# Kernel tuning notes

Hardware: AMD Instinct MI355X
Metric: run time of the kernel (lower is better)

## Reference

```python
import jax, jax.numpy as jnp
import numpy as np

B, N, S, VC, P, E, H = 8, 1024, 64, 8, 3, 64, 4
HD = E // H


def setup_inputs() -> dict:
    key = jax.random.key(0)
    ks = jax.random.split(key, 20)
    def rn(k, shape, scale=1.0):
        return jax.random.normal(k, shape, dtype=jnp.float32) * scale
    inp = {
        "s": rn(ks[0], (B, N, S)),
        "v": rn(ks[1], (B, N, VC, 3)),
        "coords": rn(ks[2], (B, N, 3)),
        # p-adic encoder: Linear(1,16) -> SiLU -> Linear(16, 64)
        "enc_w1": rn(ks[3], (16, 1), 1.0),
        "enc_b1": jnp.zeros((16,), jnp.float32),
        "enc_w2": rn(ks[4], (S, 16), 1.0 / np.sqrt(16)),
        "enc_b2": jnp.zeros((S,), jnp.float32),
        # 3 GVP layers, all with s_cat dim 72 -> s_out 64, v 8 -> 8
        "scal_w": rn(ks[5], (3, S, S + VC), 1.0 / np.sqrt(S + VC)),
        "scal_b": jnp.zeros((3, S), jnp.float32),
        "vec_w": rn(ks[6], (3, VC, VC), 1.0 / np.sqrt(VC)),
        "gate_w": rn(ks[7], (3, VC, S + VC), 1.0 / np.sqrt(S + VC)),
        "gate_b": jnp.zeros((3, VC), jnp.float32),
        # MultiheadAttention (embed 64, 4 heads)
        "in_proj_w": rn(ks[8], (3 * E, E), 1.0 / np.sqrt(E)),
        "in_proj_b": jnp.zeros((3 * E,), jnp.float32),
        "out_proj_w": rn(ks[9], (E, E), 1.0 / np.sqrt(E)),
        "out_proj_b": jnp.zeros((E,), jnp.float32),
    }
    return inp


def _padic_distance(coords):
    # pairwise diffs (B, N, N, 3)
    diff = coords[:, :, None, :] - coords[:, None, :, :]
    di = (jnp.abs(diff) * 1000.0).astype(jnp.int32)
    # valuation = max k in [1,10] with p^k | di  == count of divisible k (divisibility chain)
    cnt = jnp.zeros(di.shape, jnp.int32)
    for k in range(1, 11):
        cnt = cnt + (di % (P ** k) == 0).astype(jnp.int32)
    val = jnp.where(di > 0, cnt, 0).astype(jnp.float32).mean(-1)  # (B,N,N)
    return jnp.float32(P) ** (-val)


def reference(s, v, coords, enc_w1, enc_b1, enc_w2, enc_b2,
              scal_w, scal_b, vec_w, gate_w, gate_b,
              in_proj_w, in_proj_b, out_proj_w, out_proj_b):
    silu = jax.nn.silu
    pd = _padic_distance(coords)  # (B,N,N)
    pf = silu(pd.mean(-1, keepdims=True) @ enc_w1.T + enc_b1) @ enc_w2.T + enc_b2
    s = s + pf

    for i in range(3):
        act = i < 2  # last layer has no activations (gate always applied)
        vn = jnp.linalg.norm(v, axis=-1)               # (B,N,VC)
        sc = jnp.concatenate([s, vn], axis=-1)         # (B,N,S+VC)
        s_new = sc @ scal_w[i].T + scal_b[i]
        if act:
            s_new = silu(s_new)
        v_new = jnp.einsum('oi,bnix->bnox', vec_w[i], v)
        if act:
            v_new = v_new * jax.nn.sigmoid(jnp.linalg.norm(v_new, axis=-1, keepdims=True))
        gate = jax.nn.sigmoid(sc @ gate_w[i].T + gate_b[i])
        v_new = v_new * gate[..., None]
        if i > 0:
            s, v = s + s_new, v + v_new
        else:
            s, v = s_new, v_new

    # p-adic biased multi-head attention (additive mask = -padic_dist per head)
    qkv = s @ in_proj_w.T + in_proj_b                 # (B,N,3E)
    q, k, vv = jnp.split(qkv, 3, axis=-1)
    q = q.reshape(B, N, H, HD)
    k = k.reshape(B, N, H, HD)
    vv = vv.reshape(B, N, H, HD)
    scores = jnp.einsum('bqhd,bkhd->bhqk', q, k) / np.sqrt(HD)
    scores = scores - pd[:, None, :, :]
    attn = jax.nn.softmax(scores, axis=-1)
    o = jnp.einsum('bhqk,bkhd->bqhd', attn, vv).reshape(B, N, E)
    s = s + (o @ out_proj_w.T + out_proj_b)

    return s, v, pd
```

## Files before the change

### kernel.cpp

```cpp
#include <hip/hip_runtime.h>
#include <hip/hip_bf16.h>
#include <math.h>

#define BB 8
#define NN 1024
#define SS 64
#define VCC 8
#define EE 64
#define HH 4
#define HDD 16

#define OUT_S_OFF 0
#define OUT_V_OFF 524288
#define OUT_PD_OFF 720896

__device__ __forceinline__ int val3(int d) {
    int c = 0;
    unsigned ud = (unsigned)d;
    c += (ud % 3u == 0u);
    c += (ud % 9u == 0u);
    c += (ud % 27u == 0u);
    c += (ud % 81u == 0u);
    c += (ud % 243u == 0u);
    c += (ud % 729u == 0u);
    c += (ud % 2187u == 0u);
    c += (ud % 6561u == 0u);
    c += (ud % 19683u == 0u);
    c += (ud % 59049u == 0u);
    return d > 0 ? c : 0;
}

__device__ __forceinline__ float silu_f(float x) {
    return x / (1.0f + expf(-x));
}
__device__ __forceinline__ float sigmoid_f(float x) {
    return 1.0f / (1.0f + expf(-x));
}

#define IR 16
__global__ __launch_bounds__(256) void pd_kernel(const float* __restrict__ coords,
                                                 float* __restrict__ pd_out,
                                                 float* __restrict__ pdmean) {
    const int bi = blockIdx.x;
    const int b = bi >> 6;
    const int ibase = (bi & 63) * IR;
    const int tid = threadIdx.x;
    const float* cb = coords + (size_t)b * NN * 3;

    __shared__ float sx[1024];
    __shared__ float sy[1024];
    __shared__ float sz[1024];
    __shared__ float red[IR][4];

    for (int idx = tid; idx < 3072; idx += 256) {
        float v = cb[idx];
        int j = idx / 3;
        int c = idx - j * 3;
        float* dst = (c == 0) ? sx : (c == 1) ? sy : sz;
        dst[j] = v;
    }
    __syncthreads();

    const int j0 = tid * 4;
    float4 x4 = *(const float4*)&sx[j0];
    float4 y4 = *(const float4*)&sy[j0];
    float4 z4 = *(const float4*)&sz[j0];
    float xs[4] = {x4.x, x4.y, x4.z, x4.w};
    float ys[4] = {y4.x, y4.y, y4.z, y4.w};
    float zs[4] = {z4.x, z4.y, z4.z, z4.w};

    const float kLog2_3_over3 = 0.5283208335737187f;

    for (int ii = 0; ii < IR; ++ii) {
        const int i = ibase + ii;
        const float cx = sx[i], cy = sy[i], cz = sz[i];
        float p[4];
        float lsum = 0.0f;
        #pragma unroll
        for (int t = 0; t < 4; ++t) {
            int d0 = (int)(fabsf(cx - xs[t]) * 1000.0f);
            int d1 = (int)(fabsf(cy - ys[t]) * 1000.0f);
            int d2 = (int)(fabsf(cz - zs[t]) * 1000.0f);
            int cnt = val3(d0) + val3(d1) + val3(d2);
            p[t] = exp2f(-(float)cnt * kLog2_3_over3);
            lsum += p[t];
        }
        *(float4*)&pd_out[((size_t)(b * NN + i)) * NN + j0] =
            make_float4(p[0], p[1], p[2], p[3]);
        float x = lsum;
        #pragma unroll
        for (int off = 32; off > 0; off >>= 1) x += __shfl_xor(x, off, 64);
        if ((tid & 63) == 0) red[ii][tid >> 6] = x;
    }
    __syncthreads();
    if (tid < IR) {
        pdmean[b * NN + ibase + tid] =
            (red[tid][0] + red[tid][1] + red[tid][2] + red[tid][3]) * (1.0f / 1024.0f);
    }
}

#define GR 4
__global__ __launch_bounds__(64) void gvp_kernel(const float* __restrict__ s_in,
                           const float* __restrict__ v_in,
                           const float* __restrict__ enc_w1,
                           const float* __restrict__ enc_b1,
                           const float* __restrict__ enc_w2,
                           const float* __restrict__ enc_b2,
                           const float* __restrict__ scal_w,
                           const float* __restrict__ scal_b,
                           const float* __restrict__ vec_w,
                           const float* __restrict__ gate_w,
                           const float* __restrict__ gate_b,
                           const float* __restrict__ pdmean,
                           float* __restrict__ s_gvp,
                           float* __restrict__ v_out) {
    const int lane = threadIdx.x;
    const int rbase = blockIdx.x * GR;

    __shared__ float sc[GR][80];
    __shared__ float vbuf[GR][24];
    __shared__ float vtb[GR][24];
    __shared__ float gg[GR][8];
    __shared__ float hid[GR][16];

    #pragma unroll
    for (int r = 0; r < GR; ++r) {
        const int row = rbase + r;
        sc[r][lane] = s_in[(size_t)row * 64 + lane];
        if (lane < 24) vbuf[r][lane] = v_in[(size_t)row * 24 + lane];
        if (lane < 16) {
            float pm = pdmean[row];
            hid[r][lane] = silu_f(pm * enc_w1[lane] + enc_b1[lane]);
        }
    }
    __syncthreads();
    #pragma unroll
    for (int r = 0; r < GR; ++r) {
        float acc = enc_b2[lane];
        #pragma unroll
        for (int h = 0; h < 16; ++h) acc += hid[r][h] * enc_w2[lane * 16 + h];
        sc[r][lane] += acc;
    }
    __syncthreads();

    for (int layer = 0; layer < 3; ++layer) {
        const bool act = layer < 2;
        if (lane < 8) {
            #pragma unroll
            for (int r = 0; r < GR; ++r) {
                float x = vbuf[r][lane * 3 + 0];
                float y = vbuf[r][lane * 3 + 1];
                float z = vbuf[r][lane * 3 + 2];
                sc[r][64 + lane] = sqrtf(x * x + y * y + z * z);
            }
        }
        __syncthreads();

        float sn[GR];
        {
            float4 w4[18];
            const float4* wr = (const float4*)(scal_w + ((size_t)layer * 64 + lane) * 72);
            #pragma unroll
            for (int k = 0; k < 18; ++k) w4[k] = wr[k];
            const float sb = scal_b[layer * 64 + lane];
            #pragma unroll
            for (int r = 0; r < GR; ++r) {
                const float4* sv = (const float4*)sc[r];
                float acc = sb;
                #pragma unroll
                for (int k = 0; k < 18; ++k) {
                    float4 s4 = sv[k];
                    acc += w4[k].x * s4.x + w4[k].y * s4.y + w4[k].z * s4.z + w4[k].w * s4.w;
                }
                sn[r] = acc;
            }
        }
        if (lane < 8) {
            float4 g4[18];
            const float4* gr_ = (const float4*)(gate_w + ((size_t)layer * 8 + lane) * 72);
            #pragma unroll
            for (int k = 0; k < 18; ++k) g4[k] = gr_[k];
            const float gb = gate_b[layer * 8 + lane];
            #pragma unroll
            for (int r = 0; r < GR; ++r) {
                const float4* sv = (const float4*)sc[r];
                float acc = gb;
                #pragma unroll
                for (int k = 0; k < 18; ++k) {
                    float4 s4 = sv[k];
                    acc += g4[k].x * s4.x + g4[k].y * s4.y + g4[k].z * s4.z + g4[k].w * s4.w;
                }
                gg[r][lane] = sigmoid_f(acc);
            }
        }
        if (lane < 24) {
            const int o = lane / 3;
            const int xc = lane - o * 3;
            const float* vw = vec_w + ((size_t)layer * 8 + o) * 8;
            float vwr[8];
            #pragma unroll
            for (int ii = 0; ii < 8; ++ii) vwr[ii] = vw[ii];
            #pragma unroll
            for (int r = 0; r < GR; ++r) {
                float acc = 0.0f;
                #pragma unroll
                for (int ii = 0; ii < 8; ++ii) acc += vwr[ii] * vbuf[r][ii * 3 + xc];
                vtb[r][lane] = acc;
            }
        }
        __syncthreads();

        #pragma unroll
        for (int r = 0; r < GR; ++r) {
            float val = act ? silu_f(sn[r]) : sn[r];
            sc[r][lane] = (layer > 0) ? (sc[r][lane] + val) : val;
        }
        if (lane < 24) {
            const int o = lane / 3;
            #pragma unroll
            for (int r = 0; r < GR; ++r) {
                float val = vtb[r][lane];
                if (act) {
                    float a = vtb[r][o * 3 + 0];
                    float bb2 = vtb[r][o * 3 + 1];
                    float c2 = vtb[r][o * 3 + 2];
                    val *= sigmoid_f(sqrtf(a * a + bb2 * bb2 + c2 * c2));
                }
                val *= gg[r][o];
                vbuf[r][lane] = (layer > 0) ? (vbuf[r][lane] + val) : val;
            }
        }
        __syncthreads();
    }

    #pragma unroll
    for (int r = 0; r < GR; ++r) {
        const int row = rbase + r;
        s_gvp[(size_t)row * 64 + lane] = sc[r][lane];
        if (lane < 24) v_out[(size_t)row * 24 + lane] = vbuf[r][lane];
    }
}

#define QROWS 8
__global__ __launch_bounds__(192) void qkv_kernel(const float* __restrict__ s_gvp,
                           const float* __restrict__ w,
                           const float* __restrict__ bias,
                           float* __restrict__ q,
                           float* __restrict__ k,
                           float* __restrict__ v) {
    const int tid = threadIdx.x;
    const int rbase = blockIdx.x * QROWS;
    __shared__ float sl[QROWS][64];
    for (int idx = tid; idx < QROWS * 64; idx += 192)
        sl[idx >> 6][idx & 63] = s_gvp[(size_t)rbase * 64 + idx];
    __syncthreads();

    float4 w4[16];
    const float4* wr = (const float4*)(w + (size_t)tid * 64);
    #pragma unroll
    for (int kk = 0; kk < 16; ++kk) w4[kk] = wr[kk];
    const float bv = bias[tid];

    const int which = tid >> 6;
    const int e = tid & 63;
    const int h = e >> 4, d = e & 15;
    float* dst = (which == 0) ? q : (which == 1) ? k : v;

    #pragma unroll
    for (int r = 0; r < QROWS; ++r) {
        const float4* sv = (const float4*)sl[r];
        float acc = bv;
        #pragma unroll
        for (int kk = 0; kk < 16; ++kk) {
            float4 s4 = sv[kk];
            acc += w4[kk].x * s4.x + w4[kk].y * s4.y + w4[kk].z * s4.z + w4[kk].w * s4.w;
        }
        const int row = rbase + r;
        const int b = row >> 10, n = row & 1023;
        dst[(((size_t)(b * HH + h)) * NN + n) * HDD + d] = acc;
    }
}

__global__ __launch_bounds__(256, 2)
void attn_kernel(const float* __restrict__ q,
                 const float* __restrict__ k,
                 const float* __restrict__ v,
                 const float* __restrict__ pd,
                 float* __restrict__ po,
                 float* __restrict__ pm,
                 float* __restrict__ pl) {
    const int ks = blockIdx.x & 1;
    const int qt = (blockIdx.x >> 1) & 15;
    const int bh = blockIdx.x >> 5;
    const int b = bh >> 2;
    const int tid = threadIdx.x;
    const int kl = tid & 15;
    const int qg = tid >> 4;
    const int qbase = qt * 64 + qg * 4;

    __shared__ float kt[128][20];
    __shared__ float vt[128][20];

    float qreg[4][16];
    const float* qb_ = q + ((size_t)bh * NN + qbase) * HDD;
    #pragma unroll
    for (int i = 0; i < 4; ++i) {
        #pragma unroll
        for (int d = 0; d < 16; d += 4) {
            float4 t4 = *(const float4*)(qb_ + i * 16 + d);
            qreg[i][d] = t4.x; qreg[i][d+1] = t4.y; qreg[i][d+2] = t4.z; qreg[i][d+3] = t4.w;
        }
    }
    const float* pdr0 = pd + ((size_t)b * NN + qbase) * NN + ks * 512;

    float acc[4][16];
    #pragma unroll
    for (int i = 0; i < 4; ++i)
        #pragma unroll
        for (int d = 0; d < 16; ++d) acc[i][d] = 0.0f;
    float mrun[4] = {-INFINITY, -INFINITY, -INFINITY, -INFINITY};
    float lrun[4] = {0.0f, 0.0f, 0.0f, 0.0f};

    const float* kbase = k + ((size_t)bh * NN + ks * 512) * HDD;
    const float* vbase = v + ((size_t)bh * NN + ks * 512) * HDD;
    const float kLog2e = 1.44269504f;

    for (int tile = 0; tile < 4; ++tile) {
        __syncthreads();
        {
            const float4* kg = (const float4*)(kbase + (size_t)tile * 128 * 16);
            const float4* vg = (const float4*)(vbase + (size_t)tile * 128 * 16);
            int c0 = tid, c1 = tid + 256;
            int r0 = c0 >> 2, s0 = c0 & 3;
            int r1 = c1 >> 2, s1 = c1 & 3;
            *(float4*)&kt[r0][s0 * 4] = kg[c0];
            *(float4*)&kt[r1][s1 * 4] = kg[c1];
            *(float4*)&vt[r0][s0 * 4] = vg[c0];
            *(float4*)&vt[r1][s1 * 4] = vg[c1];
        }
        __syncthreads();

        float sc[4][8];
        #pragma unroll
        for (int m = 0; m < 8; ++m) {
            const int jt = kl + 16 * m;
            float kr[16];
            #pragma unroll
            for (int d = 0; d < 16; d += 4) {
                float4 t4 = *(const float4*)&kt[jt][d];
                kr[d] = t4.x; kr[d+1] = t4.y; kr[d+2] = t4.z; kr[d+3] = t4.w;
            }
            const int j = tile * 128 + jt;
            #pragma unroll
            for (int i = 0; i < 4; ++i) {
                float a = 0.0f;
                #pragma unroll
                for (int d = 0; d < 16; ++d) a += qreg[i][d] * kr[d];
                sc[i][m] = a * 0.25f - pdr0[(size_t)i * NN + j];
            }
        }

        #pragma unroll
        for (int i = 0; i < 4; ++i) {
            float tmax = sc[i][0];
            #pragma unroll
            for (int m = 1; m < 8; ++m) tmax = fmaxf(tmax, sc[i][m]);
            #pragma unroll
            for (int w = 1; w < 16; w <<= 1) tmax = fmaxf(tmax, __shfl_xor(tmax, w, 16));
            float mnew = fmaxf(mrun[i], tmax);
            float scale = exp2f((mrun[i] - mnew) * kLog2e);
            mrun[i] = mnew;
            lrun[i] *= scale;
            #pragma unroll
            for (int d = 0; d < 16; ++d) acc[i][d] *= scale;
            float ls = 0.0f;
            #pragma unroll
            for (int m = 0; m < 8; ++m) {
                float p = exp2f((sc[i][m] - mnew) * kLog2e);
                sc[i][m] = p;
                ls += p;
            }
            lrun[i] += ls;
        }

        #pragma unroll
        for (int m = 0; m < 8; ++m) {
            const int jt = kl + 16 * m;
            float vr[16];
            #pragma unroll
            for (int d = 0; d < 16; d += 4) {
                float4 t4 = *(const float4*)&vt[jt][d];
                vr[d] = t4.x; vr[d+1] = t4.y; vr[d+2] = t4.z; vr[d+3] = t4.w;
            }
            #pragma unroll
            for (int i = 0; i < 4; ++i) {
                const float p = sc[i][m];
                #pragma unroll
                for (int d = 0; d < 16; ++d) acc[i][d] += p * vr[d];
            }
        }
    }

    #pragma unroll
    for (int i = 0; i < 4; ++i) {
        float l = lrun[i];
        #pragma unroll
        for (int w = 1; w < 16; w <<= 1) l += __shfl_xor(l, w, 16);
        lrun[i] = l;
    }
    float outv[4] = {0.0f, 0.0f, 0.0f, 0.0f};
    #pragma unroll
    for (int i = 0; i < 4; ++i) {
        #pragma unroll
        for (int d = 0; d < 16; ++d) {
            float a = acc[i][d];
            #pragma unroll
            for (int w = 1; w < 16; w <<= 1) a += __shfl_xor(a, w, 16);
            if (kl == d) outv[i] = a;
        }
    }
    const size_t sbase = (size_t)ks * 32768 + (size_t)bh * NN + qbase;
    #pragma unroll
    for (int i = 0; i < 4; ++i) {
        po[(sbase + i) * 16 + kl] = outv[i];
        if (kl == 0) {
            pm[sbase + i] = mrun[i];
            pl[sbase + i] = lrun[i];
        }
    }
}

#define OROWS 16
__global__ __launch_bounds__(256) void outproj_kernel(const float* __restrict__ s_gvp,
                               const float* __restrict__ po,
                               const float* __restrict__ pm,
                               const float* __restrict__ pl,
                               const float* __restrict__ w,
                               const float* __restrict__ bias,
                               float* __restrict__ s_out) {
    const int tid = threadIdx.x;
    const int col = tid & 63;
    const int wq = tid >> 6;
    const int rbase = blockIdx.x * OROWS;
    __shared__ float ol[OROWS][64];
    const float kLog2e = 1.44269504f;
    for (int idx = tid; idx < OROWS * 64; idx += 256) {
        const int r = idx >> 6;
        const int c = idx & 63;
        const int row = rbase + r;
        const int b = row >> 10, n = row & 1023;
        const int h = c >> 4, d = c & 15;
        const size_t i2 = (size_t)(b * HH + h) * NN + n;
        float m0 = pm[i2], m1 = pm[32768 + i2];
        float l0 = pl[i2], l1 = pl[32768 + i2];
        float a0 = po[i2 * 16 + d], a1 = po[(32768 + i2) * 16 + d];
        float mm = fmaxf(m0, m1);
        float e0 = exp2f((m0 - mm) * kLog2e);
        float e1 = exp2f((m1 - mm) * kLog2e);
        ol[r][c] = (a0 * e0 + a1 * e1) / (l0 * e0 + l1 * e1);
    }
    __syncthreads();

    float4 w4[16];
    const float4* wr = (const float4*)(w + (size_t)col * 64);
    #pragma unroll
    for (int kk = 0; kk < 16; ++kk) w4[kk] = wr[kk];
    const float bv = bias[col];

    #pragma unroll
    for (int rr = 0; rr < OROWS / 4; ++rr) {
        const int r = wq * (OROWS / 4) + rr;
        const float4* sv = (const float4*)ol[r];
        float acc = bv;
        #pragma unroll
        for (int kk = 0; kk < 16; ++kk) {
            float4 s4 = sv[kk];
            acc += w4[kk].x * s4.x + w4[kk].y * s4.y + w4[kk].z * s4.z + w4[kk].w * s4.w;
        }
        const int row = rbase + r;
        s_out[(size_t)row * 64 + col] = s_gvp[(size_t)row * 64 + col] + acc;
    }
}

extern "C" void kernel_launch(void* const* d_in, const int* in_sizes, int n_in,
                              void* d_out, int out_size, void* d_ws, size_t ws_size,
                              hipStream_t stream) {
    const float* s_in      = (const float*)d_in[0];
    const float* v_in      = (const float*)d_in[1];
    const float* coords    = (const float*)d_in[2];
    const float* enc_w1    = (const float*)d_in[3];
    const float* enc_b1    = (const float*)d_in[4];
    const float* enc_w2    = (const float*)d_in[5];
    const float* enc_b2    = (const float*)d_in[6];
    const float* scal_w    = (const float*)d_in[7];
    const float* scal_b    = (const float*)d_in[8];
    const float* vec_w     = (const float*)d_in[9];
    const float* gate_w    = (const float*)d_in[10];
    const float* gate_b    = (const float*)d_in[11];
    const float* in_proj_w = (const float*)d_in[12];
    const float* in_proj_b = (const float*)d_in[13];
    const float* out_proj_w= (const float*)d_in[14];
    const float* out_proj_b= (const float*)d_in[15];

    float* out_s  = (float*)d_out + OUT_S_OFF;
    float* out_v  = (float*)d_out + OUT_V_OFF;
    float* out_pd = (float*)d_out + OUT_PD_OFF;

    float* ws      = (float*)d_ws;
    float* pdmean  = ws;
    float* s_gvp   = ws + 8192;
    float* qb      = s_gvp + 524288;
    float* kb      = qb + 524288;
    float* vvb     = kb + 524288;
    float* po      = vvb + 524288;
    float* pm      = po + 2 * 32768 * 16;
    float* pl      = pm + 2 * 32768;

    const int rows = BB * NN;

    pd_kernel<<<BB * (NN / IR), 256, 0, stream>>>(coords, out_pd, pdmean);
    gvp_kernel<<<rows / GR, 64, 0, stream>>>(s_in, v_in, enc_w1, enc_b1, enc_w2, enc_b2,
                                             scal_w, scal_b, vec_w, gate_w, gate_b,
                                             pdmean, s_gvp, out_v);
    qkv_kernel<<<rows / QROWS, 192, 0, stream>>>(s_gvp, in_proj_w, in_proj_b, qb, kb, vvb);
    attn_kernel<<<BB * HH * (NN / 64) * 2, 256, 0, stream>>>(qb, kb, vvb, out_pd, po, pm, pl);
    outproj_kernel<<<rows / OROWS, 256, 0, stream>>>(s_gvp, po, pm, pl,
                                                     out_proj_w, out_proj_b, out_s);
}
```

Measured before the change: 190.9 us.

## Prefetch K/V tiles into registers, parallelize gate matvec, enlarge QKV row block

The attention kernel now loads the next K/V tile from global memory into registers while the current tile is being computed, so load latency overlaps with compute. In the GVP kernel, the gate projection is spread across all 64 lanes, with each group of 8 lanes computing one output through shuffle reductions, instead of running on only 8 lanes; the gate weights are preloaded into registers. The QKV kernel now processes 16 rows per block instead of 8 to reuse the weights more. This raises register pressure and halves the QKV grid size.

```diff
diff --git a/kernel.cpp b/kernel.cpp
--- a/kernel.cpp
+++ b/kernel.cpp
@@ -123,6 +123,17 @@
     __shared__ float gg[GR][8];
     __shared__ float hid[GR][16];
 
+    const int gc = lane >> 3;
+    const int gi = lane & 7;
+
+    float gw[3][9];
+    #pragma unroll
+    for (int L = 0; L < 3; ++L) {
+        const float* gwr = gate_w + ((size_t)L * 8 + gc) * 72 + gi;
+        #pragma unroll
+        for (int t = 0; t < 9; ++t) gw[L][t] = gwr[8 * t];
+    }
+
     #pragma unroll
     for (int r = 0; r < GR; ++r) {
         const int row = rbase + r;
@@ -175,22 +186,17 @@
                 sn[r] = acc;
             }
         }
-        if (lane < 8) {
-            float4 g4[18];
-            const float4* gr_ = (const float4*)(gate_w + ((size_t)layer * 8 + lane) * 72);
-            #pragma unroll
-            for (int k = 0; k < 18; ++k) g4[k] = gr_[k];
-            const float gb = gate_b[layer * 8 + lane];
+        {
+            const float gb = gate_b[layer * 8 + gc];
             #pragma unroll
             for (int r = 0; r < GR; ++r) {
-                const float4* sv = (const float4*)sc[r];
-                float acc = gb;
+                float ga = 0.0f;
                 #pragma unroll
-                for (int k = 0; k < 18; ++k) {
-                    float4 s4 = sv[k];
-                    acc += g4[k].x * s4.x + g4[k].y * s4.y + g4[k].z * s4.z + g4[k].w * s4.w;
-                }
-                gg[r][lane] = sigmoid_f(acc);
+                for (int t = 0; t < 9; ++t) ga += gw[layer][t] * sc[r][gi + 8 * t];
+                ga += __shfl_xor(ga, 1, 8);
+                ga += __shfl_xor(ga, 2, 8);
+                ga += __shfl_xor(ga, 4, 8);
+                if (gi == 0) gg[r][gc] = sigmoid_f(ga + gb);
             }
         }
         if (lane < 24) {
@@ -241,7 +247,7 @@
     }
 }
 
-#define QROWS 8
+#define QROWS 16
 __global__ __launch_bounds__(192) void qkv_kernel(const float* __restrict__ s_gvp,
                            const float* __restrict__ w,
                            const float* __restrict__ bias,
@@ -325,20 +331,31 @@
     const float* vbase = v + ((size_t)bh * NN + ks * 512) * HDD;
     const float kLog2e = 1.44269504f;
 
+    const int r0 = tid >> 2, s0 = tid & 3;
+    const int r1 = (tid + 256) >> 2, s1 = tid & 3;
+
+    float4 kp0, kp1, vp0, vp1;
+    {
+        const float4* kg = (const float4*)kbase;
+        const float4* vg = (const float4*)vbase;
+        kp0 = kg[tid]; kp1 = kg[tid + 256];
+        vp0 = vg[tid]; vp1 = vg[tid + 256];
+    }
+
     for (int tile = 0; tile < 4; ++tile) {
         __syncthreads();
-        {
-            const float4* kg = (const float4*)(kbase + (size_t)tile * 128 * 16);
-            const float4* vg = (const float4*)(vbase + (size_t)tile * 128 * 16);
-            int c0 = tid, c1 = tid + 256;
-            int r0 = c0 >> 2, s0 = c0 & 3;
-            int r1 = c1 >> 2, s1 = c1 & 3;
-            *(float4*)&kt[r0][s0 * 4] = kg[c0];
-            *(float4*)&kt[r1][s1 * 4] = kg[c1];
-            *(float4*)&vt[r0][s0 * 4] = vg[c0];
-            *(float4*)&vt[r1][s1 * 4] = vg[c1];
-        }
+        *(float4*)&kt[r0][s0 * 4] = kp0;
+        *(float4*)&kt[r1][s1 * 4] = kp1;
+        *(float4*)&vt[r0][s0 * 4] = vp0;
+        *(float4*)&vt[r1][s1 * 4] = vp1;
         __syncthreads();
+
+        if (tile < 3) {
+            const float4* kg = (const float4*)(kbase + (size_t)(tile + 1) * 2048);
+            const float4* vg = (const float4*)(vbase + (size_t)(tile + 1) * 2048);
+            kp0 = kg[tid]; kp1 = kg[tid + 256];
+            vp0 = vg[tid]; vp1 = vg[tid + 256];
+        }
 
         float sc[4][8];
         #pragma unroll
```

Result: faster. 176.1 us (-7.8%).
